# Kernel optimization log

Measured on AMD Instinct MI355X. Metric: run time of the kernel, lower is better.

## Reference

```python
import jax, jax.numpy as jnp
import numpy as np

B, V, E, D_IN, D_OUT = 8, 10000, 160000, 128, 128
BN_EPS = 1e-5


def setup_inputs() -> dict:
    key = jax.random.key(0)
    ks = jax.random.split(key, 8)
    X = jax.random.normal(ks[0], (B, V, D_IN), dtype=jnp.float32)
    edge_attr = jax.random.normal(ks[1], (B, E), dtype=jnp.float32)
    W_node = jax.random.normal(ks[2], (D_OUT, D_IN), dtype=jnp.float32) * (1.0 / np.sqrt(D_IN))
    W_edge = jax.random.normal(ks[3], (D_OUT, 1), dtype=jnp.float32)
    W_self = jax.random.normal(ks[4], (D_OUT, D_IN), dtype=jnp.float32) * (1.0 / np.sqrt(D_IN))
    b_self = jax.random.normal(ks[5], (D_OUT,), dtype=jnp.float32) * 0.01
    gamma = jnp.ones((D_OUT,), dtype=jnp.float32)
    beta = jnp.zeros((D_OUT,), dtype=jnp.float32)
    edge_index = jax.random.randint(ks[6], (E, 2), 0, V, dtype=jnp.int32)
    return {"X": X, "edge_attr": edge_attr, "W_node": W_node, "W_edge": W_edge,
            "W_self": W_self, "b_self": b_self, "gamma": gamma, "beta": beta,
            "edge_index": edge_index}


def reference(X, edge_attr, W_node, W_edge, W_self, b_self, gamma, beta, edge_index):
    src = edge_index[:, 0]  # [E]
    dst = edge_index[:, 1]  # [E]
    # self-loop linear
    H = jnp.einsum('bvf,of->bvo', X, W_self) + b_self  # [B,V,D_OUT]
    # fused gather -> per-edge message -> scatter-add
    msg = jnp.einsum('bef,of->beo', X[:, src, :], W_node)  # [B,E,D_OUT]
    msg = msg + edge_attr[:, :, None] * W_edge[:, 0][None, None, :]
    aggregated = jnp.zeros_like(H).at[:, dst, :].add(msg)
    H = H + aggregated
    # BatchNorm1d over channel dim (training mode, biased variance over B*V)
    mean = jnp.mean(H, axis=(0, 1))
    var = jnp.var(H, axis=(0, 1))
    Hn = (H - mean) * jax.lax.rsqrt(var + BN_EPS) * gamma + beta
    return jax.nn.relu(Hn)
```

## Files before the change

### kernel.cpp

```cpp
#include <hip/hip_runtime.h>

#define B_ 8
#define V_ 10000
#define E_ 160000
#define DIN 128
#define DOUT 128
#define M_ (B_*V_)
#define NINV (1.0f/80000.0f)
#define BN_EPS 1e-5f

#define GEMM_BLOCKS 625
#define CAP 64

#define WS_CNT     0
#define WS_SUM     10000
#define WS_SUMSQ   10128
#define WS_ZERO_UNITS 10256
#define WS_S       10256
#define WS_SSRC    90256
#define WS_EAS     730256
#define WS_WPK     5850256
#define WS_XH      5866640
#define WS_AH      10986640

typedef __attribute__((ext_vector_type(2))) _Float16 half2_t;
typedef __attribute__((ext_vector_type(4))) _Float16 half4_t;
typedef __attribute__((ext_vector_type(8))) _Float16 half8_t;
typedef __attribute__((ext_vector_type(4))) float f32x4;

__device__ inline half2_t i2h(unsigned i) {
    half2_t h; __builtin_memcpy(&h, &i, 4); return h;
}
__device__ inline unsigned h2i(half2_t h) {
    unsigned i; __builtin_memcpy(&i, &h, 4); return i;
}

__global__ __launch_bounds__(256) void prep_kernel(
    const float* __restrict__ X, _Float16* __restrict__ Xh,
    const float* __restrict__ Wself, const float* __restrict__ Wnode,
    _Float16* __restrict__ Wpk,
    const int* __restrict__ EI, const float* __restrict__ EA,
    int* __restrict__ cnt, int* __restrict__ ssrc, float* __restrict__ EAs)
{
    const int blk = blockIdx.x;
    const int t = threadIdx.x;
    if (blk < 10000) {
        int idx = blk * 256 + t;
        float4 v = ((const float4*)X)[idx];
        half4_t o = { (_Float16)v.x, (_Float16)v.y, (_Float16)v.z, (_Float16)v.w };
        ((half4_t*)Xh)[idx] = o;
    } else if (blk < 10016) {
        int g = (blk - 10000) * 256 + t;
        int pair = g >> 6;
        int lane = g & 63;
        int ks = pair >> 3;
        int nt = pair & 7;
        int o = nt * 16 + (lane & 15);
        int k = ks * 32 + (lane >> 4) * 8;
        const float* wsrc = (k < 128) ? (Wself + o * 128 + k)
                                      : (Wnode + o * 128 + (k - 128));
        _Float16* dst = Wpk + ((size_t)pair * 64 + lane) * 8;
#pragma unroll
        for (int j = 0; j < 8; ++j) dst[j] = (_Float16)wsrc[j];
    } else {
        int e = (blk - 10016) * 256 + t;
        int src = EI[2 * e];
        int dst = EI[2 * e + 1];
        int slot = atomicAdd(&cnt[dst], 1);
        if (slot < CAP) {
            int p = dst * CAP + slot;
            ssrc[p] = src;
            float4 v0, v1;
            v0.x = EA[0 * E_ + e]; v0.y = EA[1 * E_ + e];
            v0.z = EA[2 * E_ + e]; v0.w = EA[3 * E_ + e];
            v1.x = EA[4 * E_ + e]; v1.y = EA[5 * E_ + e];
            v1.z = EA[6 * E_ + e]; v1.w = EA[7 * E_ + e];
            *(float4*)(EAs + (size_t)p * 8) = v0;
            *(float4*)(EAs + (size_t)p * 8 + 4) = v1;
        }
    }
}

__global__ __launch_bounds__(256) void gather_kernel(
    const _Float16* __restrict__ Xh, const float* __restrict__ EAs,
    const int* __restrict__ cnt, const int* __restrict__ ssrc,
    _Float16* __restrict__ Ah, float* __restrict__ S)
{
    const int b = blockIdx.x & 7;
    const int dblk = blockIdx.x >> 3;
    const int w = threadIdx.x >> 6;
    const int lane = threadIdx.x & 63;
    const int q = lane >> 4;
    const int sl = lane & 15;
    const int d = dblk * 4 + w;
    const int wid = b * V_ + d;
    const int deg = min(cnt[d], CAP);
    const int k0 = d * CAP;
    const _Float16* Xb = Xh + (size_t)b * V_ * DIN + sl * 8;
    half2_t a0 = (half2_t)0, a1 = (half2_t)0, a2 = (half2_t)0, a3 = (half2_t)0;
    float ea = 0.0f;
    {
        int msrc = 0;
        if (lane < deg) {
            msrc = ssrc[k0 + lane];
            ea = EAs[(size_t)(k0 + lane) * 8 + b];
        }
        int j = 0;
        for (; j + 16 <= deg; j += 16) {
#pragma unroll
            for (int u = 0; u < 4; ++u) {
                int s = __shfl(msrc, j + u * 4 + q);
                uint4 v = *(const uint4*)(Xb + (size_t)s * DIN);
                a0 += i2h(v.x); a1 += i2h(v.y); a2 += i2h(v.z); a3 += i2h(v.w);
            }
        }
        for (; j + 4 <= deg; j += 4) {
            int s = __shfl(msrc, j + q);
            uint4 v = *(const uint4*)(Xb + (size_t)s * DIN);
            a0 += i2h(v.x); a1 += i2h(v.y); a2 += i2h(v.z); a3 += i2h(v.w);
        }
        if (j < deg) {
            int s = __shfl(msrc, j + q);
            if (j + q < deg) {
                uint4 v = *(const uint4*)(Xb + (size_t)s * DIN);
                a0 += i2h(v.x); a1 += i2h(v.y); a2 += i2h(v.z); a3 += i2h(v.w);
            }
        }
    }
#pragma unroll
    for (int off = 32; off >= 16; off >>= 1) {
        a0 += i2h(__shfl_down(h2i(a0), off));
        a1 += i2h(__shfl_down(h2i(a1), off));
        a2 += i2h(__shfl_down(h2i(a2), off));
        a3 += i2h(__shfl_down(h2i(a3), off));
    }
    for (int off = 32; off; off >>= 1) ea += __shfl_down(ea, off);
    if (lane == 0) S[wid] = ea;
    if (lane < 16) {
        uint4 o;
        o.x = h2i(a0); o.y = h2i(a1); o.z = h2i(a2); o.w = h2i(a3);
        *(uint4*)(Ah + (size_t)wid * DIN + sl * 8) = o;
    }
}

template<bool STATS>
__device__ __forceinline__ void gemm_body(
    const _Float16* __restrict__ Xh, const _Float16* __restrict__ Ah,
    const _Float16* __restrict__ Wpk, const float* __restrict__ S,
    const float* __restrict__ bself, const float* __restrict__ wedge,
    int bid, int t, f32x4 (&acc)[2][8], float* cs, float* css,
    _Float16* wlds)
{
    const int wave = t >> 6;
    const int lane = t & 63;
    const int quad = lane >> 4;
    const int ln = lane & 15;
    const int rowbase = bid * 128 + wave * 32;
    const int m0 = rowbase + ln;
    const int m1 = rowbase + 16 + ln;

#pragma unroll
    for (int i = 0; i < 16; ++i) {
        int chunk = wave * 16 + i;
        __builtin_amdgcn_global_load_lds(
            (const __attribute__((address_space(1))) void*)
                ((const char*)Wpk + (size_t)chunk * 1024 + lane * 16),
            (__attribute__((address_space(3))) void*)
                ((char*)wlds + (size_t)chunk * 1024),
            16, 0, 0);
    }

    if constexpr (STATS) {
        if (t < 128) { cs[t] = 0.0f; css[t] = 0.0f; }
    }

#pragma unroll
    for (int mt = 0; mt < 2; ++mt)
#pragma unroll
        for (int nt = 0; nt < 8; ++nt) acc[mt][nt] = (f32x4){0.f, 0.f, 0.f, 0.f};

    const _Float16* X0 = Xh + (size_t)m0 * DIN + quad * 8;
    const _Float16* X1 = Xh + (size_t)m1 * DIN + quad * 8;
    const _Float16* A0 = Ah + (size_t)m0 * DIN + quad * 8;
    const _Float16* A1 = Ah + (size_t)m1 * DIN + quad * 8;

    half8_t afr[2][8];
#pragma unroll
    for (int ks = 0; ks < 4; ++ks) {
        afr[0][ks]     = *(const half8_t*)(X0 + ks * 32);
        afr[1][ks]     = *(const half8_t*)(X1 + ks * 32);
        afr[0][4 + ks] = *(const half8_t*)(A0 + ks * 32);
        afr[1][4 + ks] = *(const half8_t*)(A1 + ks * 32);
    }

    __syncthreads();

#pragma unroll
    for (int ks = 0; ks < 8; ++ks) {
#pragma unroll
        for (int nt = 0; nt < 8; ++nt) {
            half8_t bfr = *(const half8_t*)(wlds + (size_t)(ks * 8 + nt) * 512 + lane * 8);
            acc[0][nt] = __builtin_amdgcn_mfma_f32_16x16x32_f16(afr[0][ks], bfr, acc[0][nt], 0, 0, 0);
            acc[1][nt] = __builtin_amdgcn_mfma_f32_16x16x32_f16(afr[1][ks], bfr, acc[1][nt], 0, 0, 0);
        }
    }

    float bs[8], we[8];
#pragma unroll
    for (int nt = 0; nt < 8; ++nt) {
        int c = nt * 16 + ln;
        bs[nt] = bself[c];
        we[nt] = wedge[c];
    }
    float psum[8], psq[8];
    if constexpr (STATS) {
#pragma unroll
        for (int nt = 0; nt < 8; ++nt) { psum[nt] = 0.0f; psq[nt] = 0.0f; }
    }

#pragma unroll
    for (int mt = 0; mt < 2; ++mt) {
        const int rbase = rowbase + mt * 16 + quad * 4;
        float sv[4];
#pragma unroll
        for (int r = 0; r < 4; ++r) sv[r] = S[rbase + r];
#pragma unroll
        for (int nt = 0; nt < 8; ++nt) {
#pragma unroll
            for (int r = 0; r < 4; ++r) {
                float h = acc[mt][nt][r] + bs[nt] + sv[r] * we[nt];
                acc[mt][nt][r] = h;
                if constexpr (STATS) {
                    psum[nt] += h;
                    psq[nt] += h * h;
                }
            }
        }
    }
    if constexpr (STATS) {
#pragma unroll
        for (int nt = 0; nt < 8; ++nt) {
            psum[nt] += __shfl_down(psum[nt], 32);
            psum[nt] += __shfl_down(psum[nt], 16);
            psq[nt] += __shfl_down(psq[nt], 32);
            psq[nt] += __shfl_down(psq[nt], 16);
        }
        __syncthreads();
        if (lane < 16) {
#pragma unroll
            for (int nt = 0; nt < 8; ++nt) {
                atomicAdd(&cs[nt * 16 + ln], psum[nt]);
                atomicAdd(&css[nt * 16 + ln], psq[nt]);
            }
        }
        __syncthreads();
    }
}

__global__ __launch_bounds__(256) void stats_gemm_kernel(
    const _Float16* __restrict__ Xh, const _Float16* __restrict__ Ah,
    const _Float16* __restrict__ Wpk, const float* __restrict__ S,
    const float* __restrict__ bself, const float* __restrict__ wedge,
    float* __restrict__ gsum, float* __restrict__ gsumsq)
{
    __shared__ _Float16 wlds[32768];
    __shared__ float cs[128];
    __shared__ float css[128];
    const int t = threadIdx.x;
    f32x4 acc[2][8];
    gemm_body<true>(Xh, Ah, Wpk, S, bself, wedge, blockIdx.x, t, acc, cs, css,
                    wlds);
    if (t < 128) atomicAdd(&gsum[t], cs[t]);
    else atomicAdd(&gsumsq[t - 128], css[t - 128]);
}

__global__ __launch_bounds__(256) void norm_gemm_kernel(
    const _Float16* __restrict__ Xh, const _Float16* __restrict__ Ah,
    const _Float16* __restrict__ Wpk, const float* __restrict__ S,
    const float* __restrict__ bself, const float* __restrict__ wedge,
    const float* __restrict__ gsum, const float* __restrict__ gsumsq,
    const float* __restrict__ gamma, const float* __restrict__ beta,
    float* __restrict__ H)
{
    __shared__ _Float16 wlds[32768];
    const int t = threadIdx.x;
    f32x4 acc[2][8];
    gemm_body<false>(Xh, Ah, Wpk, S, bself, wedge, blockIdx.x, t, acc,
                     nullptr, nullptr, wlds);

    const int wave = t >> 6;
    const int lane = t & 63;
    const int quad = lane >> 4;
    const int ln = lane & 15;
    const int rowbase = blockIdx.x * 128 + wave * 32;
    float sc[8], sh[8];
#pragma unroll
    for (int nt = 0; nt < 8; ++nt) {
        int c = nt * 16 + ln;
        float mean = gsum[c] * NINV;
        float rstd = rsqrtf(gsumsq[c] * NINV - mean * mean + BN_EPS);
        sc[nt] = gamma[c] * rstd;
        sh[nt] = beta[c] - mean * sc[nt];
    }
#pragma unroll
    for (int mt = 0; mt < 2; ++mt) {
        const int rbase = rowbase + mt * 16 + quad * 4;
#pragma unroll
        for (int r = 0; r < 4; ++r) {
            float* Hr = H + (size_t)(rbase + r) * DOUT + ln;
#pragma unroll
            for (int nt = 0; nt < 8; ++nt)
                Hr[nt * 16] = fmaxf(acc[mt][nt][r] * sc[nt] + sh[nt], 0.0f);
        }
    }
}

extern "C" void kernel_launch(void* const* d_in, const int* in_sizes, int n_in,
                              void* d_out, int out_size, void* d_ws, size_t ws_size,
                              hipStream_t stream)
{
    const float* X      = (const float*)d_in[0];
    const float* EA     = (const float*)d_in[1];
    const float* Wnode  = (const float*)d_in[2];
    const float* Wedge  = (const float*)d_in[3];
    const float* Wself  = (const float*)d_in[4];
    const float* bself  = (const float*)d_in[5];
    const float* gamma  = (const float*)d_in[6];
    const float* beta   = (const float*)d_in[7];
    const int*   EI     = (const int*)d_in[8];

    int*   wsI    = (int*)d_ws;
    float* wsF    = (float*)d_ws;
    int*   cnt    = wsI + WS_CNT;
    float* gsum   = wsF + WS_SUM;
    float* gsumsq = wsF + WS_SUMSQ;
    float* S      = wsF + WS_S;
    int*   ssrc   = wsI + WS_SSRC;
    float* EAs    = wsF + WS_EAS;
    _Float16* Wpk = (_Float16*)(wsI + WS_WPK);
    _Float16* Xh  = (_Float16*)(wsI + WS_XH);
    _Float16* Ah  = (_Float16*)(wsI + WS_AH);
    float* H      = (float*)d_out;

    hipMemsetAsync(d_ws, 0, (size_t)WS_ZERO_UNITS * 4, stream);

    prep_kernel<<<10641, 256, 0, stream>>>(X, Xh, Wself, Wnode, Wpk, EI, EA,
                                           cnt, ssrc, EAs);

    gather_kernel<<<M_ / 4, 256, 0, stream>>>(Xh, EAs, cnt, ssrc, Ah, S);

    stats_gemm_kernel<<<GEMM_BLOCKS, 256, 0, stream>>>(Xh, Ah, Wpk, S, bself,
                                                       Wedge, gsum, gsumsq);
    norm_gemm_kernel<<<GEMM_BLOCKS, 256, 0, stream>>>(Xh, Ah, Wpk, S, bself,
                                                      Wedge, gsum, gsumsq,
                                                      gamma, beta, H);
}
```

Measured before the change: 200.8 us.

## Store pre-BN activations in fp16 instead of recomputing GEMM in norm pass

Before this change the GEMM ran twice, once to accumulate BatchNorm statistics and once to normalize. Now the single GEMM pass writes the pre-normalization H as fp16 into workspace, reusing the EAs region, while it accumulates the statistics. A separate elementwise kernel then applies the BN scale/shift and ReLU. This removes the second GEMM and its reloads of Xh, Ah and W, but adds a 20 MB fp16 write and read and rounds H to fp16 before normalization.

New measurement: 198.1 us. No clear change (-1.4%).

```diff
diff --git a/kernel.cpp b/kernel.cpp
--- a/kernel.cpp
+++ b/kernel.cpp
@@ -19,6 +19,7 @@
 #define WS_S       10256
 #define WS_SSRC    90256
 #define WS_EAS     730256
+#define WS_HH      730256
 #define WS_WPK     5850256
 #define WS_XH      5866640
 #define WS_AH      10986640
@@ -143,19 +144,22 @@
     }
 }
 
-template<bool STATS>
-__device__ __forceinline__ void gemm_body(
+__global__ __launch_bounds__(256) void gemm_stats_kernel(
     const _Float16* __restrict__ Xh, const _Float16* __restrict__ Ah,
     const _Float16* __restrict__ Wpk, const float* __restrict__ S,
     const float* __restrict__ bself, const float* __restrict__ wedge,
-    int bid, int t, f32x4 (&acc)[2][8], float* cs, float* css,
-    _Float16* wlds)
-{
+    _Float16* __restrict__ Hh, float* __restrict__ gsum,
+    float* __restrict__ gsumsq)
+{
+    __shared__ _Float16 wlds[32768];
+    __shared__ float cs[128];
+    __shared__ float css[128];
+    const int t = threadIdx.x;
     const int wave = t >> 6;
     const int lane = t & 63;
     const int quad = lane >> 4;
     const int ln = lane & 15;
-    const int rowbase = bid * 128 + wave * 32;
+    const int rowbase = blockIdx.x * 128 + wave * 32;
     const int m0 = rowbase + ln;
     const int m1 = rowbase + 16 + ln;
 
@@ -170,10 +174,9 @@
             16, 0, 0);
     }
 
-    if constexpr (STATS) {
-        if (t < 128) { cs[t] = 0.0f; css[t] = 0.0f; }
-    }
-
+    if (t < 128) { cs[t] = 0.0f; css[t] = 0.0f; }
+
+    f32x4 acc[2][8];
 #pragma unroll
     for (int mt = 0; mt < 2; ++mt)
 #pragma unroll
@@ -213,10 +216,8 @@
         we[nt] = wedge[c];
     }
     float psum[8], psq[8];
-    if constexpr (STATS) {
-#pragma unroll
-        for (int nt = 0; nt < 8; ++nt) { psum[nt] = 0.0f; psq[nt] = 0.0f; }
-    }
+#pragma unroll
+    for (int nt = 0; nt < 8; ++nt) { psum[nt] = 0.0f; psq[nt] = 0.0f; }
 
 #pragma unroll
     for (int mt = 0; mt < 2; ++mt) {
@@ -225,93 +226,78 @@
 #pragma unroll
         for (int r = 0; r < 4; ++r) sv[r] = S[rbase + r];
 #pragma unroll
+        for (int r = 0; r < 4; ++r) {
+            _Float16* Hr = Hh + (size_t)(rbase + r) * DOUT + ln;
+#pragma unroll
+            for (int nt = 0; nt < 8; ++nt) {
+                float h = acc[mt][nt][r] + bs[nt] + sv[r] * we[nt];
+                Hr[nt * 16] = (_Float16)h;
+                psum[nt] += h;
+                psq[nt] += h * h;
+            }
+        }
+    }
+#pragma unroll
+    for (int nt = 0; nt < 8; ++nt) {
+        psum[nt] += __shfl_down(psum[nt], 32);
+        psum[nt] += __shfl_down(psum[nt], 16);
+        psq[nt] += __shfl_down(psq[nt], 32);
+        psq[nt] += __shfl_down(psq[nt], 16);
+    }
+    __syncthreads();
+    if (lane < 16) {
+#pragma unroll
         for (int nt = 0; nt < 8; ++nt) {
-#pragma unroll
-            for (int r = 0; r < 4; ++r) {
-                float h = acc[mt][nt][r] + bs[nt] + sv[r] * we[nt];
-                acc[mt][nt][r] = h;
-                if constexpr (STATS) {
-                    psum[nt] += h;
-                    psq[nt] += h * h;
-                }
-            }
-        }
-    }
-    if constexpr (STATS) {
-#pragma unroll
-        for (int nt = 0; nt < 8; ++nt) {
-            psum[nt] += __shfl_down(psum[nt], 32);
-            psum[nt] += __shfl_down(psum[nt], 16);
-            psq[nt] += __shfl_down(psq[nt], 32);
-            psq[nt] += __shfl_down(psq[nt], 16);
-        }
-        __syncthreads();
-        if (lane < 16) {
-#pragma unroll
-            for (int nt = 0; nt < 8; ++nt) {
-                atomicAdd(&cs[nt * 16 + ln], psum[nt]);
-                atomicAdd(&css[nt * 16 + ln], psq[nt]);
-            }
-        }
-        __syncthreads();
-    }
-}
-
-__global__ __launch_bounds__(256) void stats_gemm_kernel(
-    const _Float16* __restrict__ Xh, const _Float16* __restrict__ Ah,
-    const _Float16* __restrict__ Wpk, const float* __restrict__ S,
-    const float* __restrict__ bself, const float* __restrict__ wedge,
-    float* __restrict__ gsum, float* __restrict__ gsumsq)
-{
-    __shared__ _Float16 wlds[32768];
-    __shared__ float cs[128];
-    __shared__ float css[128];
-    const int t = threadIdx.x;
-    f32x4 acc[2][8];
-    gemm_body<true>(Xh, Ah, Wpk, S, bself, wedge, blockIdx.x, t, acc, cs, css,
-                    wlds);
+            atomicAdd(&cs[nt * 16 + ln], psum[nt]);
+            atomicAdd(&css[nt * 16 + ln], psq[nt]);
+        }
+    }
+    __syncthreads();
     if (t < 128) atomicAdd(&gsum[t], cs[t]);
     else atomicAdd(&gsumsq[t - 128], css[t - 128]);
 }
 
-__global__ __launch_bounds__(256) void norm_gemm_kernel(
-    const _Float16* __restrict__ Xh, const _Float16* __restrict__ Ah,
-    const _Float16* __restrict__ Wpk, const float* __restrict__ S,
-    const float* __restrict__ bself, const float* __restrict__ wedge,
+__global__ __launch_bounds__(256) void norm_relu_kernel(
+    const _Float16* __restrict__ Hh, float* __restrict__ H,
     const float* __restrict__ gsum, const float* __restrict__ gsumsq,
-    const float* __restrict__ gamma, const float* __restrict__ beta,
-    float* __restrict__ H)
-{
-    __shared__ _Float16 wlds[32768];
-    const int t = threadIdx.x;
-    f32x4 acc[2][8];
-    gemm_body<false>(Xh, Ah, Wpk, S, bself, wedge, blockIdx.x, t, acc,
-                     nullptr, nullptr, wlds);
-
-    const int wave = t >> 6;
-    const int lane = t & 63;
-    const int quad = lane >> 4;
-    const int ln = lane & 15;
-    const int rowbase = blockIdx.x * 128 + wave * 32;
-    float sc[8], sh[8];
-#pragma unroll
-    for (int nt = 0; nt < 8; ++nt) {
-        int c = nt * 16 + ln;
-        float mean = gsum[c] * NINV;
-        float rstd = rsqrtf(gsumsq[c] * NINV - mean * mean + BN_EPS);
-        sc[nt] = gamma[c] * rstd;
-        sh[nt] = beta[c] - mean * sc[nt];
-    }
-#pragma unroll
-    for (int mt = 0; mt < 2; ++mt) {
-        const int rbase = rowbase + mt * 16 + quad * 4;
-#pragma unroll
-        for (int r = 0; r < 4; ++r) {
-            float* Hr = H + (size_t)(rbase + r) * DOUT + ln;
-#pragma unroll
-            for (int nt = 0; nt < 8; ++nt)
-                Hr[nt * 16] = fmaxf(acc[mt][nt][r] * sc[nt] + sh[nt], 0.0f);
-        }
+    const float* __restrict__ gamma, const float* __restrict__ beta)
+{
+    const int total = M_ * DOUT / 8;
+    for (int idx = blockIdx.x * 256 + threadIdx.x; idx < total;
+         idx += gridDim.x * 256) {
+        int o8 = (idx & 15) * 8;
+        float4 s0 = *(const float4*)(gsum + o8);
+        float4 s1 = *(const float4*)(gsum + o8 + 4);
+        float4 q0 = *(const float4*)(gsumsq + o8);
+        float4 q1 = *(const float4*)(gsumsq + o8 + 4);
+        float4 g0 = *(const float4*)(gamma + o8);
+        float4 g1 = *(const float4*)(gamma + o8 + 4);
+        float4 b0 = *(const float4*)(beta + o8);
+        float4 b1 = *(const float4*)(beta + o8 + 4);
+        float sc[8], sh[8];
+        float sv[8] = {s0.x, s0.y, s0.z, s0.w, s1.x, s1.y, s1.z, s1.w};
+        float qv[8] = {q0.x, q0.y, q0.z, q0.w, q1.x, q1.y, q1.z, q1.w};
+        float gv[8] = {g0.x, g0.y, g0.z, g0.w, g1.x, g1.y, g1.z, g1.w};
+        float bv[8] = {b0.x, b0.y, b0.z, b0.w, b1.x, b1.y, b1.z, b1.w};
+#pragma unroll
+        for (int j = 0; j < 8; ++j) {
+            float mean = sv[j] * NINV;
+            float rstd = rsqrtf(qv[j] * NINV - mean * mean + BN_EPS);
+            sc[j] = gv[j] * rstd;
+            sh[j] = bv[j] - mean * sc[j];
+        }
+        half8_t hv = ((const half8_t*)Hh)[idx];
+        float4 o0, o1;
+        o0.x = fmaxf((float)hv[0] * sc[0] + sh[0], 0.0f);
+        o0.y = fmaxf((float)hv[1] * sc[1] + sh[1], 0.0f);
+        o0.z = fmaxf((float)hv[2] * sc[2] + sh[2], 0.0f);
+        o0.w = fmaxf((float)hv[3] * sc[3] + sh[3], 0.0f);
+        o1.x = fmaxf((float)hv[4] * sc[4] + sh[4], 0.0f);
+        o1.y = fmaxf((float)hv[5] * sc[5] + sh[5], 0.0f);
+        o1.z = fmaxf((float)hv[6] * sc[6] + sh[6], 0.0f);
+        o1.w = fmaxf((float)hv[7] * sc[7] + sh[7], 0.0f);
+        ((float4*)H)[idx * 2]     = o0;
+        ((float4*)H)[idx * 2 + 1] = o1;
     }
 }
 
@@ -337,6 +323,7 @@
     float* S      = wsF + WS_S;
     int*   ssrc   = wsI + WS_SSRC;
     float* EAs    = wsF + WS_EAS;
+    _Float16* Hh  = (_Float16*)(wsI + WS_HH);
     _Float16* Wpk = (_Float16*)(wsI + WS_WPK);
     _Float16* Xh  = (_Float16*)(wsI + WS_XH);
     _Float16* Ah  = (_Float16*)(wsI + WS_AH);
@@ -349,9 +336,8 @@
 
     gather_kernel<<<M_ / 4, 256, 0, stream>>>(Xh, EAs, cnt, ssrc, Ah, S);
 
-    stats_gemm_kernel<<<GEMM_BLOCKS, 256, 0, stream>>>(Xh, Ah, Wpk, S, bself,
-                                                       Wedge, gsum, gsumsq);
-    norm_gemm_kernel<<<GEMM_BLOCKS, 256, 0, stream>>>(Xh, Ah, Wpk, S, bself,
-                                                      Wedge, gsum, gsumsq,
-                                                      gamma, beta, H);
-}
+    gemm_stats_kernel<<<GEMM_BLOCKS, 256, 0, stream>>>(Xh, Ah, Wpk, S, bself,
+                                                       Wedge, Hh, gsum, gsumsq);
+
+    norm_relu_kernel<<<2048, 256, 0, stream>>>(Hh, H, gsum, gsumsq, gamma, beta);
+}
```
